# Kernel tuning notes

Hardware: AMD Instinct MI355X
Metric: run time of the kernel (lower is better)

## Reference

```python
import jax, jax.numpy as jnp
import numpy as np

H = 1024  # hidden_size


def _cell(x, W, b):
    # x: [S, B, D_in]; W: [4H, D_in]; b: [4H]
    # One big batched matmul over all timesteps (no recurrence exists).
    gates = jnp.einsum('sbd,gd->sbg', x, W) + b  # [S, B, 4H]
    i, f, g, o = jnp.split(gates, 4, axis=-1)
    i = jax.nn.sigmoid(i)
    g = jnp.tanh(g)
    o = jax.nn.sigmoid(o)
    c = i * g
    h = o * jnp.tanh(c)
    return h, c


def setup_inputs() -> dict:
    key = jax.random.key(0)
    ks = jax.random.split(key, 9)
    S, B, D = 2048, 8, 1024
    s = 1.0 / np.sqrt(D)
    s2 = 1.0 / np.sqrt(2 * H)
    return {
        'x': jax.random.normal(ks[0], (S, B, D), dtype=jnp.float32),
        'W_f0': jax.random.uniform(ks[1], (4 * H, D), jnp.float32, -s, s),
        'b_f0': jax.random.uniform(ks[2], (4 * H,), jnp.float32, -s, s),
        'W_b0': jax.random.uniform(ks[3], (4 * H, D), jnp.float32, -s, s),
        'b_b0': jax.random.uniform(ks[4], (4 * H,), jnp.float32, -s, s),
        'W_f1': jax.random.uniform(ks[5], (4 * H, 2 * H), jnp.float32, -s2, s2),
        'b_f1': jax.random.uniform(ks[6], (4 * H,), jnp.float32, -s2, s2),
        'W_b1': jax.random.uniform(ks[7], (4 * H, 2 * H), jnp.float32, -s2, s2),
        'b_b1': jax.random.uniform(ks[8], (4 * H,), jnp.float32, -s2, s2),
    }


def reference(x, W_f0, b_f0, W_b0, b_b0, W_f1, b_f1, W_b1, b_b1):
    out = x
    h_ns, c_ns = [], []
    for (Wf, bf, Wb, bb) in [(W_f0, b_f0, W_b0, b_b0), (W_f1, b_f1, W_b1, b_b1)]:
        h_f, c_f = _cell(out, Wf, bf)  # forward direction
        h_b, c_b = _cell(out, Wb, bb)  # backward direction (same per-t math)
        out = jnp.concatenate([h_f, h_b], axis=-1)  # [S, B, 2H]
        # forward final state is at t = S-1; backward final state at t = 0
        h_ns += [h_f[-1], h_b[0]]
        c_ns += [c_f[-1], c_b[0]]
    h_n = jnp.stack(h_ns, axis=0)  # [num_layers*2, B, H]
    c_n = jnp.stack(c_ns, axis=0)
    return out, h_n, c_n
```

## Files before the change

kernel.cpp:

```cpp
#include <hip/hip_runtime.h>
#include <hip/hip_bf16.h>

#define S_LEN 2048
#define BATCH 8
#define HID   1024
#define NP    3072
#define MROWS 16384

using bf16x8 = __attribute__((ext_vector_type(8))) short;
using f32x16 = __attribute__((ext_vector_type(16))) float;

__device__ __forceinline__ unsigned short f2b(float f) {
  unsigned int u = __builtin_bit_cast(unsigned int, f);
  u += 0x7fffu + ((u >> 16) & 1u);
  return (unsigned short)(u >> 16);
}

__device__ __forceinline__ float sigf(float x) {
  return 1.f / (1.f + __expf(-x));
}
__device__ __forceinline__ float tanh_f(float x) {
  return 2.f / (1.f + __expf(-2.f * x)) - 1.f;
}

__device__ __forceinline__ void load_lds16(const void* g, void* l) {
  __builtin_amdgcn_global_load_lds(
      (const __attribute__((address_space(1))) void*)g,
      (__attribute__((address_space(3))) void*)(unsigned int)(unsigned long long)l,
      16, 0, 0);
}

#define MEMFENCE asm volatile("" ::: "memory")
#define BARRIER  do { MEMFENCE; __builtin_amdgcn_s_barrier(); MEMFENCE; } while (0)

__device__ __forceinline__ void pack_w_dev(const float* __restrict__ W,
                                           unsigned short* __restrict__ Wp,
                                           int id, int Kshift, int ntshift) {
  const int l = id & 63;
  const int q = id >> 6;
  const int c = q % 24;
  const int q24 = q / 24;
  const int t  = q24 & ((1 << ntshift) - 1);
  const int bn = q24 >> ntshift;
  const int nf = c >> 1, ks = c & 1;
  const int gate = nf % 3, hgrp = nf / 3;
  const int og = (gate == 0) ? 0 : (gate == 1) ? 2 : 3;
  const int row = og * 1024 + (bn * 4 + hgrp) * 32 + (l & 31);
  const int k   = t * 32 + ks * 16 + (l >> 5) * 8;
  const float* s = W + ((long)row << Kshift) + k;
  const float4 v0 = *reinterpret_cast<const float4*>(s);
  const float4 v1 = *reinterpret_cast<const float4*>(s + 4);
  uint4 o;
  o.x = (unsigned)f2b(v0.x) | ((unsigned)f2b(v0.y) << 16);
  o.y = (unsigned)f2b(v0.z) | ((unsigned)f2b(v0.w) << 16);
  o.z = (unsigned)f2b(v1.x) | ((unsigned)f2b(v1.y) << 16);
  o.w = (unsigned)f2b(v1.z) | ((unsigned)f2b(v1.w) << 16);
  *reinterpret_cast<uint4*>(Wp + (long)id * 8) = o;
}

__global__ void prep(const float* __restrict__ x, unsigned short* __restrict__ x_bf,
                     const float* __restrict__ Wf0, const float* __restrict__ Wb0,
                     const float* __restrict__ Wf1, const float* __restrict__ Wb1,
                     unsigned short* __restrict__ pf0, unsigned short* __restrict__ pb0,
                     unsigned short* __restrict__ pf1, unsigned short* __restrict__ pb1,
                     const float* __restrict__ bf0, const float* __restrict__ bb0,
                     const float* __restrict__ bf1, const float* __restrict__ bb1,
                     float* __restrict__ bpf0, float* __restrict__ bpb0,
                     float* __restrict__ bpf1, float* __restrict__ bpb1) {
  const int blk = blockIdx.x;
  const int tid = threadIdx.x;
  if (blk < 16384) {
    const int i = blk * 256 + tid;
    const float4 v = reinterpret_cast<const float4*>(x)[i];
    ushort4 u;
    u.x = f2b(v.x); u.y = f2b(v.y); u.z = f2b(v.z); u.w = f2b(v.w);
    reinterpret_cast<ushort4*>(x_bf)[i] = u;
  } else if (blk < 17920) {
    pack_w_dev(Wf0, pf0, (blk - 16384) * 256 + tid, 10, 5);
  } else if (blk < 19456) {
    pack_w_dev(Wb0, pb0, (blk - 17920) * 256 + tid, 10, 5);
  } else if (blk < 22528) {
    pack_w_dev(Wf1, pf1, (blk - 19456) * 256 + tid, 11, 6);
  } else if (blk < 25600) {
    pack_w_dev(Wb1, pb1, (blk - 22528) * 256 + tid, 11, 6);
  } else {
    const int r = blk - 25600;
    const int which = r / 12;
    const int np = (r % 12) * 256 + tid;
    const float* bs = which == 0 ? bf0 : which == 1 ? bb0 : which == 2 ? bf1 : bb1;
    float* bd       = which == 0 ? bpf0 : which == 1 ? bpb0 : which == 2 ? bpf1 : bpb1;
    const int c32 = np / 96, rem = np % 96;
    const int gate = rem >> 5, hl = rem & 31;
    const int og = (gate == 0) ? 0 : (gate == 1) ? 2 : 3;
    bd[np] = bs[og * 1024 + c32 * 32 + hl];
  }
}

#define MFMAOP(a_, b_, c_) \
  c_ = __builtin_amdgcn_mfma_f32_32x32x16_bf16(a_, b_, c_, 0, 0, 0)

template <int MODE>
__global__ void __launch_bounds__(512, 2)
lstm_gemm(const unsigned short* __restrict__ A,
          const unsigned short* __restrict__ PF,
          const unsigned short* __restrict__ PB,
          const float* __restrict__ bpF, const float* __restrict__ bpB,
          int K,
          unsigned short* __restrict__ out_bf, float* __restrict__ out_f,
          float* __restrict__ hn, float* __restrict__ cn) {
  __shared__ __align__(16) char lds[81920];

  const int dir = blockIdx.z;
  const unsigned short* __restrict__ Wp = dir ? PB : PF;
  const float* __restrict__ bp = dir ? bpB : bpF;
  const int bm = blockIdx.y;
  const int bn = blockIdx.x;

  const int tid  = threadIdx.x;
  const int wid  = tid >> 6;
  const int lane = tid & 63;
  const int wm   = wid >> 2;
  const int wn   = wid & 3;
  const int l31  = lane & 31;
  const int b5   = lane >> 5;

  const int  nt = K >> 5;
  const long K2 = (long)K * 2;

  const char *srcA0, *srcA1;
  int dA0, dA1;
  {
    const int c0 = wid, c1 = wid + 8;
    srcA0 = (const char*)A + ((long)(bm * 256 + (c0 >> 1) * 32 + l31)) * K2
            + (c0 & 1) * 32 + b5 * 16;
    srcA1 = (const char*)A + ((long)(bm * 256 + (c1 >> 1) * 32 + l31)) * K2
            + (c1 & 1) * 32 + b5 * 16;
    dA0 = c0 * 1024; dA1 = c1 * 1024;
  }
  const char* srcB = (const char*)Wp + (long)bn * nt * 24576 + wid * 1024 + lane * 16;
  const int dB0 = 16384 + wid * 1024;

#define ISSUE(T) do {                                              \
    char* d_ = lds + ((T) & 1) * 40960;                            \
    const long ta_ = (long)(T) * 64;                               \
    const long tb_ = (long)(T) * 24576;                            \
    load_lds16(srcA0 + ta_, d_ + dA0);                             \
    load_lds16(srcA1 + ta_, d_ + dA1);                             \
    load_lds16(srcB + tb_,         d_ + dB0);                      \
    load_lds16(srcB + tb_ + 8192,  d_ + dB0 + 8192);               \
    load_lds16(srcB + tb_ + 16384, d_ + dB0 + 16384);              \
  } while (0)

  const int abase = wm * 8192 + lane * 16;
  const int bbase = 16384 + wn * 6144 + lane * 16;

  f32x16 acc[4][3];
#pragma unroll
  for (int i = 0; i < 4; ++i)
#pragma unroll
    for (int j = 0; j < 3; ++j)
      acc[i][j] = (f32x16)(0.f);

#define KSTEP(BUF, S) do {                                         \
    bf16x8 A0 = *(const bf16x8*)((BUF) + abase +        (S)*1024); \
    bf16x8 A1 = *(const bf16x8*)((BUF) + abase + 2048 + (S)*1024); \
    bf16x8 A2 = *(const bf16x8*)((BUF) + abase + 4096 + (S)*1024); \
    bf16x8 A3 = *(const bf16x8*)((BUF) + abase + 6144 + (S)*1024); \
    bf16x8 B0 = *(const bf16x8*)((BUF) + bbase +        (S)*1024); \
    bf16x8 B1 = *(const bf16x8*)((BUF) + bbase + 2048 + (S)*1024); \
    bf16x8 B2 = *(const bf16x8*)((BUF) + bbase + 4096 + (S)*1024); \
    __builtin_amdgcn_s_setprio(1);                                 \
    MFMAOP(A0, B0, acc[0][0]); MFMAOP(A1, B0, acc[1][0]);          \
    MFMAOP(A2, B0, acc[2][0]); MFMAOP(A3, B0, acc[3][0]);          \
    MFMAOP(A0, B1, acc[0][1]); MFMAOP(A1, B1, acc[1][1]);          \
    MFMAOP(A2, B1, acc[2][1]); MFMAOP(A3, B1, acc[3][1]);          \
    MFMAOP(A0, B2, acc[0][2]); MFMAOP(A1, B2, acc[1][2]);          \
    MFMAOP(A2, B2, acc[2][2]); MFMAOP(A3, B2, acc[3][2]);          \
    __builtin_amdgcn_s_setprio(0);                                 \
  } while (0)

  ISSUE(0);
  asm volatile("s_waitcnt vmcnt(0)" ::: "memory");
  BARRIER;

#pragma unroll 1
  for (int t = 0; t < nt; ++t) {
    if (t + 1 < nt) { ISSUE(t + 1); }
    const char* buf = lds + (t & 1) * 40960;
    KSTEP(buf, 0);
    KSTEP(buf, 1);
    asm volatile("s_waitcnt vmcnt(0)" ::: "memory");
    BARRIER;
  }
#undef KSTEP
#undef ISSUE

  const int c32  = bn * 4 + wn;
  const int h    = c32 * 32 + l31;
  const int outcol = dir * HID + h;
  const float bi = bp[c32 * 96 + l31];
  const float bg = bp[c32 * 96 + 32 + l31];
  const float bo = bp[c32 * 96 + 64 + l31];
  const int Lidx = MODE * 2 + dir;
  const int mrow0 = bm * 256 + wm * 128 + b5 * 4;

#pragma unroll
  for (int mf = 0; mf < 4; ++mf) {
#pragma unroll
    for (int r = 0; r < 16; ++r) {
      const int m = mrow0 + mf * 32 + (r & 3) + 8 * (r >> 2);
      const float iv = acc[mf][0][r] + bi;
      const float gv = acc[mf][1][r] + bg;
      const float ov = acc[mf][2][r] + bo;
      const float is = sigf(iv);
      const float gt = tanh_f(gv);
      const float os = sigf(ov);
      const float c  = is * gt;
      const float hv = os * tanh_f(c);
      if (MODE == 0) {
        out_bf[(long)m * 2048 + outcol] = f2b(hv);
      } else {
        out_f[(long)m * 2048 + outcol] = hv;
      }
      const bool wst = (dir == 0) ? (m >= (S_LEN - 1) * BATCH) : (m < BATCH);
      if (wst) {
        const int b = (dir == 0) ? (m - (S_LEN - 1) * BATCH) : m;
        hn[((long)Lidx * BATCH + b) * HID + h] = hv;
        cn[((long)Lidx * BATCH + b) * HID + h] = c;
      }
    }
  }
}

extern "C" void kernel_launch(void* const* d_in, const int* in_sizes, int n_in,
                              void* d_out, int out_size, void* d_ws, size_t ws_size,
                              hipStream_t stream) {
  const float* x    = (const float*)d_in[0];
  const float* W_f0 = (const float*)d_in[1];
  const float* b_f0 = (const float*)d_in[2];
  const float* W_b0 = (const float*)d_in[3];
  const float* b_b0 = (const float*)d_in[4];
  const float* W_f1 = (const float*)d_in[5];
  const float* b_f1 = (const float*)d_in[6];
  const float* W_b1 = (const float*)d_in[7];
  const float* b_b1 = (const float*)d_in[8];

  float* out = (float*)d_out;
  float* hn  = out + (long)MROWS * 2048;
  float* cn  = hn + 4 * BATCH * HID;

  unsigned short* x_bf  = (unsigned short*)d_ws;
  unsigned short* out1  = x_bf + (long)MROWS * 1024;
  unsigned short* wp_f0 = out1 + (long)MROWS * 2048;
  unsigned short* wp_b0 = wp_f0 + (long)NP * 1024;
  unsigned short* wp_f1 = wp_b0 + (long)NP * 1024;
  unsigned short* wp_b1 = wp_f1 + (long)NP * 2048;
  float* bp_f0 = (float*)(wp_b1 + (long)NP * 2048);
  float* bp_b0 = bp_f0 + NP;
  float* bp_f1 = bp_b0 + NP;
  float* bp_b1 = bp_f1 + NP;

  prep<<<25648, 256, 0, stream>>>(x, x_bf, W_f0, W_b0, W_f1, W_b1,
                                  wp_f0, wp_b0, wp_f1, wp_b1,
                                  b_f0, b_b0, b_f1, b_b1,
                                  bp_f0, bp_b0, bp_f1, bp_b1);

  dim3 grid(NP / 384, MROWS / 256, 2);
  lstm_gemm<0><<<grid, 512, 0, stream>>>(x_bf, wp_f0, wp_b0, bp_f0, bp_b0, 1024,
                                         out1, nullptr, hn, cn);
  lstm_gemm<1><<<grid, 512, 0, stream>>>(out1, wp_f1, wp_b1, bp_f1, bp_b1, 2048,
                                         nullptr, out, hn, cn);
}
```

Measured before the change: 687.8 us.

## Triple-buffer LDS with ping-pong register prefetch and swizzled block order

```diff
diff --git a/kernel.cpp b/kernel.cpp
--- a/kernel.cpp
+++ b/kernel.cpp
@@ -32,6 +32,7 @@
 
 #define MEMFENCE asm volatile("" ::: "memory")
 #define BARRIER  do { MEMFENCE; __builtin_amdgcn_s_barrier(); MEMFENCE; } while (0)
+#define SCHED0   __builtin_amdgcn_sched_barrier(0)
 
 __device__ __forceinline__ void pack_w_dev(const float* __restrict__ W,
                                            unsigned short* __restrict__ Wp,
@@ -99,6 +100,40 @@
 #define MFMAOP(a_, b_, c_) \
   c_ = __builtin_amdgcn_mfma_f32_32x32x16_bf16(a_, b_, c_, 0, 0, 0)
 
+#define READS(P, KS, A0_,A1_,A2_,A3_, B0_,B1_,B2_) do {           \
+    A0_ = *(const bf16x8*)((P) + abase_r          + (KS)*1024);   \
+    A1_ = *(const bf16x8*)((P) + abase_r + 2048   + (KS)*1024);   \
+    A2_ = *(const bf16x8*)((P) + abase_r + 4096   + (KS)*1024);   \
+    A3_ = *(const bf16x8*)((P) + abase_r + 6144   + (KS)*1024);   \
+    B0_ = *(const bf16x8*)((P) + bbase_r          + (KS)*1024);   \
+    B1_ = *(const bf16x8*)((P) + bbase_r + 2048   + (KS)*1024);   \
+    B2_ = *(const bf16x8*)((P) + bbase_r + 4096   + (KS)*1024);   \
+  } while (0)
+
+#define MF12(A0_,A1_,A2_,A3_, B0_,B1_,B2_) do {                   \
+    __builtin_amdgcn_s_setprio(1);                                \
+    MFMAOP(A0_,B0_,acc[0][0]); MFMAOP(A1_,B0_,acc[1][0]);         \
+    MFMAOP(A2_,B0_,acc[2][0]); MFMAOP(A3_,B0_,acc[3][0]);         \
+    MFMAOP(A0_,B1_,acc[0][1]); MFMAOP(A1_,B1_,acc[1][1]);         \
+    MFMAOP(A2_,B1_,acc[2][1]); MFMAOP(A3_,B1_,acc[3][1]);         \
+    MFMAOP(A0_,B2_,acc[0][2]); MFMAOP(A1_,B2_,acc[1][2]);         \
+    MFMAOP(A2_,B2_,acc[2][2]); MFMAOP(A3_,B2_,acc[3][2]);         \
+    __builtin_amdgcn_s_setprio(0);                                \
+  } while (0)
+
+#define STG0(T, DB) do {                                          \
+    const long ta_ = (long)(T) * 64;                              \
+    const long tb_ = (long)(T) * 24576;                           \
+    load_lds16(srcA0 + ta_, (DB) + dA0);                          \
+    load_lds16(srcA1 + ta_, (DB) + dA1);                          \
+    load_lds16(srcB  + tb_, (DB) + dB0);                          \
+  } while (0)
+#define STG1(T, DB) do {                                          \
+    const long tb_ = (long)(T) * 24576;                           \
+    load_lds16(srcB + tb_ + 8192,  (DB) + dB0 + 8192);            \
+    load_lds16(srcB + tb_ + 16384, (DB) + dB0 + 16384);           \
+  } while (0)
+
 template <int MODE>
 __global__ void __launch_bounds__(512, 2)
 lstm_gemm(const unsigned short* __restrict__ A,
@@ -108,13 +143,15 @@
           int K,
           unsigned short* __restrict__ out_bf, float* __restrict__ out_f,
           float* __restrict__ hn, float* __restrict__ cn) {
-  __shared__ __align__(16) char lds[81920];
+  __shared__ __align__(16) char lds[122880];
 
   const int dir = blockIdx.z;
   const unsigned short* __restrict__ Wp = dir ? PB : PF;
   const float* __restrict__ bp = dir ? bpB : bpF;
-  const int bm = blockIdx.y;
-  const int bn = blockIdx.x;
+
+  const int dflat = blockIdx.x + (blockIdx.y << 3);
+  const int bm = (dflat & 7) + ((dflat >> 6) << 3);
+  const int bn = (dflat >> 3) & 7;
 
   const int tid  = threadIdx.x;
   const int wid  = tid >> 6;
@@ -127,32 +164,17 @@
   const int  nt = K >> 5;
   const long K2 = (long)K * 2;
 
-  const char *srcA0, *srcA1;
-  int dA0, dA1;
-  {
-    const int c0 = wid, c1 = wid + 8;
-    srcA0 = (const char*)A + ((long)(bm * 256 + (c0 >> 1) * 32 + l31)) * K2
-            + (c0 & 1) * 32 + b5 * 16;
-    srcA1 = (const char*)A + ((long)(bm * 256 + (c1 >> 1) * 32 + l31)) * K2
-            + (c1 & 1) * 32 + b5 * 16;
-    dA0 = c0 * 1024; dA1 = c1 * 1024;
-  }
-  const char* srcB = (const char*)Wp + (long)bn * nt * 24576 + wid * 1024 + lane * 16;
+  const char* srcA0 = (const char*)A + ((long)(bm * 256 + (wid >> 1) * 32 + l31)) * K2
+                      + (wid & 1) * 32 + b5 * 16;
+  const char* srcA1 = (const char*)A + ((long)(bm * 256 + ((wid + 8) >> 1) * 32 + l31)) * K2
+                      + ((wid + 8) & 1) * 32 + b5 * 16;
+  const char* srcB  = (const char*)Wp + (long)bn * nt * 24576 + wid * 1024 + lane * 16;
+  const int dA0 = wid * 1024;
+  const int dA1 = (wid + 8) * 1024;
   const int dB0 = 16384 + wid * 1024;
 
-#define ISSUE(T) do {                                              \
-    char* d_ = lds + ((T) & 1) * 40960;                            \
-    const long ta_ = (long)(T) * 64;                               \
-    const long tb_ = (long)(T) * 24576;                            \
-    load_lds16(srcA0 + ta_, d_ + dA0);                             \
-    load_lds16(srcA1 + ta_, d_ + dA1);                             \
-    load_lds16(srcB + tb_,         d_ + dB0);                      \
-    load_lds16(srcB + tb_ + 8192,  d_ + dB0 + 8192);               \
-    load_lds16(srcB + tb_ + 16384, d_ + dB0 + 16384);              \
-  } while (0)
-
-  const int abase = wm * 8192 + lane * 16;
-  const int bbase = 16384 + wn * 6144 + lane * 16;
+  const int abase_r = wm * 8192 + lane * 16;
+  const int bbase_r = 16384 + wn * 6144 + lane * 16;
 
   f32x16 acc[4][3];
 #pragma unroll
@@ -161,39 +183,65 @@
     for (int j = 0; j < 3; ++j)
       acc[i][j] = (f32x16)(0.f);
 
-#define KSTEP(BUF, S) do {                                         \
-    bf16x8 A0 = *(const bf16x8*)((BUF) + abase +        (S)*1024); \
-    bf16x8 A1 = *(const bf16x8*)((BUF) + abase + 2048 + (S)*1024); \
-    bf16x8 A2 = *(const bf16x8*)((BUF) + abase + 4096 + (S)*1024); \
-    bf16x8 A3 = *(const bf16x8*)((BUF) + abase + 6144 + (S)*1024); \
-    bf16x8 B0 = *(const bf16x8*)((BUF) + bbase +        (S)*1024); \
-    bf16x8 B1 = *(const bf16x8*)((BUF) + bbase + 2048 + (S)*1024); \
-    bf16x8 B2 = *(const bf16x8*)((BUF) + bbase + 4096 + (S)*1024); \
-    __builtin_amdgcn_s_setprio(1);                                 \
-    MFMAOP(A0, B0, acc[0][0]); MFMAOP(A1, B0, acc[1][0]);          \
-    MFMAOP(A2, B0, acc[2][0]); MFMAOP(A3, B0, acc[3][0]);          \
-    MFMAOP(A0, B1, acc[0][1]); MFMAOP(A1, B1, acc[1][1]);          \
-    MFMAOP(A2, B1, acc[2][1]); MFMAOP(A3, B1, acc[3][1]);          \
-    MFMAOP(A0, B2, acc[0][2]); MFMAOP(A1, B2, acc[1][2]);          \
-    MFMAOP(A2, B2, acc[2][2]); MFMAOP(A3, B2, acc[3][2]);          \
-    __builtin_amdgcn_s_setprio(0);                                 \
-  } while (0)
-
-  ISSUE(0);
+  char* p0 = lds;
+  char* p1 = lds + 40960;
+  char* p2 = lds + 81920;
+
+  bf16x8 eA0, eA1, eA2, eA3, eB0, eB1, eB2;
+  bf16x8 oA0, oA1, oA2, oA3, oB0, oB1, oB2;
+
+  STG0(0, p0); STG1(0, p0);
+  STG0(1, p1); STG1(1, p1);
+  asm volatile("s_waitcnt vmcnt(5)" ::: "memory");
+  SCHED0;
+  BARRIER;
+  READS(p0, 0, eA0, eA1, eA2, eA3, eB0, eB1, eB2);
+
+#pragma unroll 1
+  for (int t = 0; t < nt - 2; ++t) {
+    READS(p0, 1, oA0, oA1, oA2, oA3, oB0, oB1, oB2);
+    STG0(t + 2, p2);
+    asm volatile("s_waitcnt vmcnt(3)" ::: "memory");
+    SCHED0;
+    BARRIER;
+    SCHED0;
+    MF12(eA0, eA1, eA2, eA3, eB0, eB1, eB2);
+    SCHED0;
+    BARRIER;
+    READS(p1, 0, eA0, eA1, eA2, eA3, eB0, eB1, eB2);
+    STG1(t + 2, p2);
+    SCHED0;
+    BARRIER;
+    SCHED0;
+    MF12(oA0, oA1, oA2, oA3, oB0, oB1, oB2);
+    SCHED0;
+    BARRIER;
+    char* tp = p0; p0 = p1; p1 = p2; p2 = tp;
+  }
+
+  READS(p0, 1, oA0, oA1, oA2, oA3, oB0, oB1, oB2);
   asm volatile("s_waitcnt vmcnt(0)" ::: "memory");
-  BARRIER;
-
-#pragma unroll 1
-  for (int t = 0; t < nt; ++t) {
-    if (t + 1 < nt) { ISSUE(t + 1); }
-    const char* buf = lds + (t & 1) * 40960;
-    KSTEP(buf, 0);
-    KSTEP(buf, 1);
-    asm volatile("s_waitcnt vmcnt(0)" ::: "memory");
-    BARRIER;
-  }
-#undef KSTEP
-#undef ISSUE
+  SCHED0;
+  BARRIER;
+  SCHED0;
+  MF12(eA0, eA1, eA2, eA3, eB0, eB1, eB2);
+  SCHED0;
+  BARRIER;
+  READS(p1, 0, eA0, eA1, eA2, eA3, eB0, eB1, eB2);
+  SCHED0;
+  BARRIER;
+  SCHED0;
+  MF12(oA0, oA1, oA2, oA3, oB0, oB1, oB2);
+  SCHED0;
+  BARRIER;
+  { char* tp = p0; p0 = p1; p1 = p2; p2 = tp; }
+
+  READS(p0, 1, oA0, oA1, oA2, oA3, oB0, oB1, oB2);
+  SCHED0;
+  BARRIER;
+  SCHED0;
+  MF12(eA0, eA1, eA2, eA3, eB0, eB1, eB2);
+  MF12(oA0, oA1, oA2, oA3, oB0, oB1, oB2);
 
   const int c32  = bn * 4 + wn;
   const int h    = c32 * 32 + l31;
```

New measurement: 1.953 ms. 2.84x slower.
